# Kernel tuning notes

Measured on AMD Instinct MI355X. Metric: run time of the kernel, lower is better.

## Reference

```python
import jax, jax.numpy as jnp
import numpy as np
jax.config.update("jax_enable_x64", True)  # int64 hash codes for lattice keys

N_KPTS = 32768
C = 61      # feature channels; f-MLP input dim is C+3 = 64
D = 64      # disp-distribution channels
D_LAT = 8   # last f-layer output -> permutohedral position dim

# large odd 62-bit multipliers for the lattice-key hash (wraps mod 2^64)
_MULTS = np.array([2654435761405764093, 1181783497276652981,
                   3202034522624059733, 2685821657736338717,
                   1876998521354586173, 1481765933965188213,
                   2549297995355413921, 3373259426345127233], dtype=np.int64)


def _hcode(k, mults):
    return jnp.sum(k.astype(jnp.int64) * mults, axis=-1)


def _pl_filter(pos, vals):
    """Permutohedral lattice splat -> blur -> slice (approx. Gaussian filter).
    pos: (N, d) float32 lattice positions, vals: (N, vd) float32 values."""
    N, d = pos.shape
    vd = vals.shape[1]
    M = N * (d + 1)  # fixed-size hash table (every point touches d+1 vertices)
    # --- elevate onto hyperplane H_d in R^{d+1} ---
    scale = np.float32(np.sqrt(2.0 / 3.0) * (d + 1)) / np.sqrt(
        np.arange(1, d + 1, dtype=np.float32) * np.arange(2, d + 2, dtype=np.float32))
    E = np.zeros((d + 1, d), dtype=np.float32)
    E[0, :] = 1.0
    for i in range(1, d + 1):
        E[i, i - 1] = -float(i)
        E[i, i:] = 1.0
    elevated = (pos * jnp.asarray(scale, jnp.float32)) @ jnp.asarray(E).T  # (N, d+1)
    # --- nearest zero-colored lattice point and simplex ranks ---
    rem0 = jnp.floor(elevated / (d + 1) + 0.5) * (d + 1)
    sum_val = jnp.round(jnp.sum(rem0, -1) / (d + 1)).astype(jnp.int32)
    diff = elevated - rem0
    rank = jnp.argsort(jnp.argsort(-diff, axis=-1), axis=-1).astype(jnp.int32) + sum_val[:, None]
    lo = rank < 0
    hi = rank > d
    rem0 = rem0 + jnp.where(lo, float(d + 1), 0.0) - jnp.where(hi, float(d + 1), 0.0)
    rank = rank + jnp.where(lo, d + 1, 0) - jnp.where(hi, d + 1, 0)
    # --- barycentric coordinates ---
    t = (elevated - rem0) / (d + 1)
    rows = jnp.arange(N)[:, None]
    bary = jnp.zeros((N, d + 2), jnp.float32)
    bary = bary.at[rows, d - rank].add(t)
    bary = bary.at[rows, d + 1 - rank].add(-t)
    bary = bary.at[:, 0].add(1.0 + bary[:, d + 1])
    w = bary[:, :d + 1]  # (N, d+1) vertex weights
    # --- simplex vertex keys (first d coords; full key sums to 0) ---
    canonical = np.zeros((d + 1, d + 1), np.int32)
    for r in range(d + 1):
        canonical[r, :d + 1 - r] = r
        canonical[r, d + 1 - r:] = r - (d + 1)
    keys = rem0.astype(jnp.int32)[None, :, :d] + jnp.asarray(canonical)[:, rank[:, :d]]  # (d+1,N,d)
    # --- hash table via sorted unique codes (jit-safe fixed size) ---
    mults = jnp.asarray(_MULTS[:d])
    codes = _hcode(keys, mults).reshape(M)
    uniq, inv = jnp.unique(codes, return_inverse=True, size=M,
                           fill_value=jnp.iinfo(jnp.int64).max)
    inv = inv.reshape(M)
    # --- splat ---
    wv = (w.T[:, :, None] * vals[None]).reshape(M, vd)
    lat = jax.ops.segment_sum(wv, inv, num_segments=M)  # (M, vd)
    occ = jax.ops.segment_sum(jnp.ones((M,), jnp.float32), inv, num_segments=M) > 0
    ukeys = jnp.zeros((M, d), jnp.int32).at[inv].set(keys.reshape(M, d))
    # --- blur along each of the d+1 lattice directions ---
    for j in range(d + 1):
        off = np.ones(d + 1, np.int32)
        off[j] = -d
        o = jnp.asarray(off[:d])
        def _nbr(sign, lat=lat):
            c = _hcode(ukeys + sign * o, mults)
            i = jnp.clip(jnp.searchsorted(uniq, c), 0, M - 1)
            ok = (jnp.take(uniq, i) == c) & jnp.take(occ, i)
            return jnp.where(ok[:, None], jnp.take(lat, i, axis=0), 0.0)
        lat = jnp.where(occ[:, None], 0.5 * lat + 0.25 * (_nbr(1) + _nbr(-1)), lat)
    # --- slice ---
    alpha = 1.0 / (1.0 + 2.0 ** (-d))
    return jnp.sum(w.T[:, :, None] * jnp.take(lat, inv, axis=0).reshape(d + 1, N, vd), 0) * alpha


def _layernorm2(x, g, b):
    # LayerNorm(normalized_shape=(N, K)): stats over the last TWO dims jointly
    mu = jnp.mean(x, axis=(-2, -1), keepdims=True)
    var = jnp.mean((x - mu) ** 2, axis=(-2, -1), keepdims=True)
    return (x - mu) * jax.lax.rsqrt(var + 1e-5) * g + b


def setup_inputs() -> dict:
    key = jax.random.key(0)
    ks = jax.random.split(key, 16)
    f32 = jnp.float32
    rn = lambda k, shape, s=1.0: jax.random.normal(k, shape, dtype=f32) * s
    inp = {
        "kpts": rn(ks[0], (1, N_KPTS, 3)),
        "disps_distr": rn(ks[1], (1, N_KPTS, D)),
        "feats": rn(ks[2], (1, N_KPTS, C)),
    }
    i = 3
    for b in range(2):
        inp[f"Wd{b}0"] = rn(ks[i], (D, D), 0.05); i += 1
        inp[f"bd{b}0"] = jnp.zeros((D,), f32)
        inp[f"Wd{b}1"] = rn(ks[i], (D, D), 0.05); i += 1
        inp[f"bd{b}1"] = jnp.zeros((D,), f32)
        inp[f"Wf{b}"] = rn(ks[i], (C + 3, D_LAT), 0.1); i += 1
        inp[f"bf{b}"] = jnp.zeros((D_LAT,), f32)
        inp[f"g{b}"] = jnp.ones((N_KPTS, D_LAT), f32)
        inp[f"be{b}"] = jnp.zeros((N_KPTS, D_LAT), f32)
    return inp


def reference(kpts, disps_distr, feats, Wd00, bd00, Wd01, bd01, Wf0, bf0, g0, be0,
              Wd10, bd10, Wd11, bd11, Wf1, bf1, g1, be1):
    fk = jnp.concatenate([kpts, feats], axis=-1)  # (1, N, C+3)
    x = jnp.reshape(disps_distr, (1, N_KPTS, -1))
    blocks = [(Wd00, bd00, Wd01, bd01, Wf0, bf0, g0, be0),
              (Wd10, bd10, Wd11, bd11, Wf1, bf1, g1, be1)]
    for (Wd0, bd0, Wd1, bd1, Wf, bf, g, be) in blocks:
        x = jax.nn.relu(x @ Wd0 + bd0)   # d-layer 0
        x = jax.nn.relu(x @ Wd1 + bd1)   # d-layer 1
        # only the LAST f-layer output is used by the torch code (feats_kpts is never updated)
        pos = _layernorm2(jax.nn.relu(fk @ Wf + bf), g, be)  # (1, N, 8)
        x = _pl_filter(pos[0], x[0])[None]
    return x
```

## Files before the change

### kernel.cpp

```cpp
#include <hip/hip_runtime.h>
#include <hip/hip_bf16.h>
#include <hip/hip_fp16.h>
#include <stdint.h>

typedef unsigned long long u64;

#define NK 32768
#define DL 8
#define DP1 9
#define MT (NK*DP1)
#define HBITS 19
#define HSIZE (1u<<HBITS)
#define HMASK (HSIZE-1)
#define EMPTY_CODE 0xFFFFFFFFFFFFFFFFULL
#define NBLK 1152
#define HBLK (HSIZE/256)
#define CAP 32
#define MAXHUB 16384

__device__ __constant__ u64 c_mults[8] = {
    2654435761405764093ULL, 1181783497276652981ULL, 3202034522624059733ULL,
    2685821657736338717ULL, 1876998521354586173ULL, 1481765933965188213ULL,
    2549297995355413921ULL, 3373259426345127233ULL};

__device__ __forceinline__ unsigned int hmix(u64 x) {
    x ^= x >> 33; x *= 0xff51afd7ed558ccdULL;
    x ^= x >> 33; x *= 0xc4ceb9fe1a85ec53ULL;
    x ^= x >> 33;
    return (unsigned int)x & HMASK;
}

__device__ __forceinline__ u64 dir_delta(int j) {
    u64 s = 0;
    #pragma unroll
    for (int k = 0; k < 8; k++) s += c_mults[k];
    return (j == 8) ? s : (s - 9ULL * c_mults[j]);
}

__device__ __forceinline__ float ldf(const void* p, int i, int bf) {
    if (bf) return __bfloat162float(((const __hip_bfloat16*)p)[i]);
    return ((const float*)p)[i];
}

__global__ void k_detect(const unsigned* __restrict__ g0w, int* __restrict__ flag) {
    if (threadIdx.x == 0) {
        int f = 1;
        for (int i = 0; i < 8; i++) if (g0w[i] != 0x3F803F80u) f = 0;
        *flag = f;
    }
}

__global__ __launch_bounds__(256) void k_mlp(const void* __restrict__ xin, int use_df_in,
    const void* __restrict__ W0, const void* __restrict__ B0,
    const void* __restrict__ W1, const void* __restrict__ B1,
    float* __restrict__ xout, const int* __restrict__ df, double* __restrict__ stats) {
    __shared__ float w0[64*64], w1[64*64], xs[16][64], y1[16][64];
    int bf = *df;
    int bfin = use_df_in ? bf : 0;
    int tid = threadIdx.x;
    int row0 = blockIdx.x * 16;
    if (blockIdx.x == 0 && tid == 0) { stats[0] = 0.0; stats[1] = 0.0; }
    for (int i = tid; i < 4096; i += 256) { w0[i] = ldf(W0, i, bf); w1[i] = ldf(W1, i, bf); }
    for (int i = tid; i < 1024; i += 256) xs[i>>6][i&63] = ldf(xin, row0*64 + i, bfin);
    __syncthreads();
    int rb = tid >> 6, col = tid & 63;
    float b0c = ldf(B0, col, bf);
    float a0 = b0c, a1 = b0c, a2 = b0c, a3 = b0c;
    #pragma unroll
    for (int k = 0; k < 64; k++) {
        float w = w0[k*64+col];
        a0 = fmaf(xs[rb   ][k], w, a0);
        a1 = fmaf(xs[rb+ 4][k], w, a1);
        a2 = fmaf(xs[rb+ 8][k], w, a2);
        a3 = fmaf(xs[rb+12][k], w, a3);
    }
    y1[rb   ][col] = fmaxf(a0, 0.f);
    y1[rb+ 4][col] = fmaxf(a1, 0.f);
    y1[rb+ 8][col] = fmaxf(a2, 0.f);
    y1[rb+12][col] = fmaxf(a3, 0.f);
    __syncthreads();
    float b1c = ldf(B1, col, bf);
    a0 = b1c; a1 = b1c; a2 = b1c; a3 = b1c;
    #pragma unroll
    for (int k = 0; k < 64; k++) {
        float w = w1[k*64+col];
        a0 = fmaf(y1[rb   ][k], w, a0);
        a1 = fmaf(y1[rb+ 4][k], w, a1);
        a2 = fmaf(y1[rb+ 8][k], w, a2);
        a3 = fmaf(y1[rb+12][k], w, a3);
    }
    xout[(row0+rb   )*64 + col] = fmaxf(a0, 0.f);
    xout[(row0+rb+ 4)*64 + col] = fmaxf(a1, 0.f);
    xout[(row0+rb+ 8)*64 + col] = fmaxf(a2, 0.f);
    xout[(row0+rb+12)*64 + col] = fmaxf(a3, 0.f);
}

__global__ __launch_bounds__(256) void k_pos(const void* __restrict__ kpts,
    const void* __restrict__ feats, const void* __restrict__ Wf,
    const void* __restrict__ Bf, float* __restrict__ pos_pre,
    double* __restrict__ stats, const int* __restrict__ df) {
    __shared__ float wf[64*8];
    __shared__ float fk[32][65];
    __shared__ float red[256], red2[256];
    int bf = *df;
    int tid = threadIdx.x;
    int n0 = blockIdx.x * 32;
    for (int i = tid; i < 512; i += 256) wf[i] = ldf(Wf, i, bf);
    for (int i = tid; i < 32*64; i += 256) {
        int pt = i >> 6, k = i & 63, n = n0 + pt;
        fk[pt][k] = (k < 3) ? ldf(kpts, n*3 + k, bf) : ldf(feats, n*61 + (k-3), bf);
    }
    __syncthreads();
    int pt = tid >> 3, j = tid & 7, n = n0 + pt;
    float acc = ldf(Bf, j, bf);
    #pragma unroll
    for (int k = 0; k < 64; k++) acc = fmaf(fk[pt][k], wf[k*8+j], acc);
    acc = fmaxf(acc, 0.f);
    pos_pre[n*8 + j] = acc;
    red[tid] = acc; red2[tid] = acc * acc;
    __syncthreads();
    for (int s = 128; s > 0; s >>= 1) {
        if (tid < s) { red[tid] += red[tid+s]; red2[tid] += red2[tid+s]; }
        __syncthreads();
    }
    if (tid == 0) { atomicAdd(&stats[0], (double)red[0]); atomicAdd(&stats[1], (double)red2[0]); }
}

__global__ __launch_bounds__(256) void k_embed(const float* __restrict__ pos_pre,
    const double* __restrict__ stats, const void* __restrict__ g,
    const void* __restrict__ be, float* __restrict__ wgt,
    u64* __restrict__ pcodes, int* __restrict__ cnt, int* __restrict__ cnt2,
    int* __restrict__ hubid, const int* __restrict__ df) {
    int bf = *df;
    int n = blockIdx.x * 256 + threadIdx.x;
    if (n >= NK) return;
    const double inv_cnt = 1.0 / (double)(NK * DL);
    double mud = stats[0] * inv_cnt;
    double vard = stats[1] * inv_cnt - mud * mud;
    float mu = (float)mud;
    float rs = rsqrtf((float)vard + 1e-5f);
    const float scale[8] = {
        5.196152422706632f, 3.0f, 2.1213203435596424f, 1.643167672515498f,
        1.3416407864998738f, 1.1338934190276817f, 0.9819805060619657f, 0.8660254037844386f};
    float c[8];
    #pragma unroll
    for (int k = 0; k < 8; k++) {
        float v = pos_pre[n*8 + k];
        float p = (v - mu) * rs * ldf(g, n*8 + k, bf) + ldf(be, n*8 + k, bf);
        c[k] = p * scale[k];
    }
    float sufa[9]; sufa[8] = 0.f;
    #pragma unroll
    for (int k = 7; k >= 0; k--) sufa[k] = sufa[k+1] + c[k];
    float elev[9];
    elev[0] = sufa[0];
    #pragma unroll
    for (int i = 1; i < 9; i++) elev[i] = sufa[i] - (float)i * c[i-1];
    int ri[9], sumv = 0;
    float diff[9];
    #pragma unroll
    for (int i = 0; i < 9; i++) {
        ri[i] = (int)floorf(elev[i] / 9.0f + 0.5f);
        sumv += ri[i];
        diff[i] = elev[i] - 9.f * (float)ri[i];
    }
    int rank[9];
    #pragma unroll
    for (int i = 0; i < 9; i++) {
        int r = 0;
        #pragma unroll
        for (int j = 0; j < 9; j++)
            r += (diff[j] > diff[i]) || ((diff[j] == diff[i]) && (j < i));
        rank[i] = r + sumv;
    }
    #pragma unroll
    for (int i = 0; i < 9; i++) {
        if (rank[i] < 0)      { rank[i] += 9; ri[i] += 1; }
        else if (rank[i] > 8) { rank[i] -= 9; ri[i] -= 1; }
    }
    float t[9];
    #pragma unroll
    for (int i = 0; i < 9; i++) t[i] = (elev[i] - 9.f * (float)ri[i]) / 9.f;
    float bary[10];
    #pragma unroll
    for (int i = 0; i < 10; i++) bary[i] = 0.f;
    #pragma unroll
    for (int i = 0; i < 9; i++) { bary[8 - rank[i]] += t[i]; bary[9 - rank[i]] -= t[i]; }
    bary[0] += 1.f + bary[9];
    for (int r = 0; r < 9; r++) {
        u64 code = 0;
        #pragma unroll
        for (int k = 0; k < 8; k++) {
            int key = 9 * ri[k] + ((rank[k] <= 8 - r) ? r : (r - 9));
            code += (u64)(long long)key * c_mults[k];
        }
        int m = n * 9 + r;
        wgt[m] = bary[r];
        pcodes[m] = code;
        cnt[m] = 0;
        cnt2[m] = 0;
        hubid[m] = -1;
    }
}

__global__ __launch_bounds__(256) void k_insert(const u64* __restrict__ pcodes,
    u64* __restrict__ htab_code, unsigned int* __restrict__ ppos) {
    int m = blockIdx.x * 256 + threadIdx.x;
    if (m >= MT) return;
    u64 code = pcodes[m];
    unsigned int pos = hmix(code);
    for (;;) {
        u64 cc = htab_code[pos];
        if (cc == code) break;
        if (cc == EMPTY_CODE) {
            u64 old = atomicCAS(&htab_code[pos], EMPTY_CODE, code);
            if (old == EMPTY_CODE || old == code) break;
        }
        pos = (pos + 1) & HMASK;
    }
    ppos[m] = pos;
}

__global__ __launch_bounds__(256) void k_occ(const u64* __restrict__ htab_code,
    int* __restrict__ bocc) {
    __shared__ int wcnt[4];
    unsigned int i = blockIdx.x * 256 + threadIdx.x;
    bool occ = (htab_code[i] != EMPTY_CODE);
    u64 mask = __ballot(occ);
    int lane = threadIdx.x & 63;
    if (lane == 0) wcnt[threadIdx.x >> 6] = __popcll(mask);
    __syncthreads();
    if (threadIdx.x == 0) bocc[blockIdx.x] = wcnt[0] + wcnt[1] + wcnt[2] + wcnt[3];
}

__global__ __launch_bounds__(256) void k_occscan(int* __restrict__ bocc,
    int* __restrict__ counter, int* __restrict__ nhub) {
    __shared__ int s[256];
    __shared__ int carry;
    int t = threadIdx.x;
    if (t == 0) { carry = 0; *nhub = 0; }
    __syncthreads();
    for (int c = 0; c < HBLK / 256; c++) {
        int i = c * 256 + t;
        int v = bocc[i];
        s[t] = v; __syncthreads();
        for (int off = 1; off < 256; off <<= 1) {
            int a = (t >= off) ? s[t-off] : 0;
            __syncthreads();
            s[t] += a;
            __syncthreads();
        }
        int cl = carry;
        bocc[i] = s[t] - v + cl;
        __syncthreads();
        if (t == 0) carry = cl + s[255];
        __syncthreads();
    }
    if (t == 0) *counter = carry;
}

__global__ __launch_bounds__(256) void k_assign2(const u64* __restrict__ htab_code,
    const int* __restrict__ bocc, int* __restrict__ htab_slot,
    u64* __restrict__ slot_code) {
    __shared__ int wbase[4];
    unsigned int i = blockIdx.x * 256 + threadIdx.x;
    u64 cde = htab_code[i];
    bool occ = (cde != EMPTY_CODE);
    int lane = threadIdx.x & 63;
    int wid  = threadIdx.x >> 6;
    u64 mask = __ballot(occ);
    int prefix = __popcll(mask & ((1ULL << lane) - 1ULL));
    if (lane == 0) wbase[wid] = __popcll(mask);
    __syncthreads();
    if (threadIdx.x == 0) {
        int run = bocc[blockIdx.x];
        for (int w = 0; w < 4; w++) { int c = wbase[w]; wbase[w] = run; run += c; }
    }
    __syncthreads();
    if (occ) {
        int s = wbase[wid] + prefix;
        htab_slot[i] = s;
        slot_code[s] = cde;
    }
}

__global__ __launch_bounds__(256) void k_nbr(const u64* __restrict__ slot_code,
    const u64* __restrict__ htab_code, const int* __restrict__ htab_slot,
    const int* __restrict__ counter, int2* __restrict__ nbr) {
    int idx = blockIdx.x * 256 + threadIdx.x;
    if (idx >= 9 * MT) return;
    int j = idx / MT;
    int sl = idx - j * MT;
    int count = *counter;
    if (sl >= count) return;
    u64 dj = dir_delta(j);
    u64 code = slot_code[sl];
    int res[2];
    #pragma unroll
    for (int s = 0; s < 2; s++) {
        u64 cde = code + (s ? (u64)(0ULL - dj) : dj);
        unsigned int pos = hmix(cde);
        int r = -1;
        for (;;) {
            u64 cc = htab_code[pos];
            if (cc == cde) { r = htab_slot[pos]; break; }
            if (cc == EMPTY_CODE) break;
            pos = (pos + 1) & HMASK;
        }
        res[s] = r;
    }
    nbr[j * MT + sl] = make_int2(res[0], res[1]);
}

__global__ __launch_bounds__(256) void k_lookup(const unsigned int* __restrict__ ppos,
    const int* __restrict__ htab_slot, int* __restrict__ sidx, int* __restrict__ cnt) {
    int m = blockIdx.x * 256 + threadIdx.x;
    if (m >= MT) return;
    int s = htab_slot[ppos[m]];
    sidx[m] = s;
    atomicAdd(&cnt[s], 1);
}

__global__ __launch_bounds__(256) void k_scan1(const int* __restrict__ cnt,
    int* __restrict__ exbuf, int* __restrict__ bsum,
    int* __restrict__ hublist, int* __restrict__ hubid, int* __restrict__ nhub) {
    __shared__ int s[256];
    int t = threadIdx.x;
    int i = blockIdx.x * 256 + t;
    int v = cnt[i];
    if (v > CAP) {
        int h = atomicAdd(nhub, 1);
        if (h < MAXHUB) { hublist[h] = i; hubid[i] = h; }
    }
    s[t] = v; __syncthreads();
    for (int off = 1; off < 256; off <<= 1) {
        int a = (t >= off) ? s[t-off] : 0;
        __syncthreads();
        s[t] += a;
        __syncthreads();
    }
    exbuf[i] = s[t] - v;
    if (t == 255) bsum[blockIdx.x] = s[255];
}

__global__ __launch_bounds__(256) void k_scan2(int* __restrict__ bsum) {
    __shared__ int s[256];
    __shared__ int carry;
    int t = threadIdx.x;
    if (t == 0) carry = 0;
    __syncthreads();
    for (int c = 0; c < (NBLK + 255) / 256; c++) {
        int i = c * 256 + t;
        int v = (i < NBLK) ? bsum[i] : 0;
        s[t] = v; __syncthreads();
        for (int off = 1; off < 256; off <<= 1) {
            int a = (t >= off) ? s[t-off] : 0;
            __syncthreads();
            s[t] += a;
            __syncthreads();
        }
        int cl = carry;
        if (i < NBLK) bsum[i] = s[t] - v + cl;
        __syncthreads();
        if (t == 0) carry = cl + s[255];
        __syncthreads();
    }
}

__global__ __launch_bounds__(256) void k_scatter(const int* __restrict__ sidx,
    const int* __restrict__ exbuf, const int* __restrict__ bsum,
    int* __restrict__ cnt2, int* __restrict__ list) {
    int m = blockIdx.x * 256 + threadIdx.x;
    if (m < MT) {
        int s = sidx[m];
        int ofs = atomicAdd(&cnt2[s], 1);
        list[exbuf[s] + bsum[s >> 8] + ofs] = m;
    }
}

__global__ __launch_bounds__(256) void k_splat_a(const float* __restrict__ xbuf,
    const float* __restrict__ wgt, const int* __restrict__ exbuf,
    const int* __restrict__ bsum, const int* __restrict__ cnt,
    const int* __restrict__ list, __half* __restrict__ val,
    const int* __restrict__ counter) {
    int count = *counter;
    int sl = blockIdx.x * 8 + (threadIdx.x >> 5);
    int lane = threadIdx.x & 31;
    if (sl >= count) return;
    int c = cnt[sl];
    if (c > CAP) return;
    int st = exbuf[sl] + bsum[sl >> 8];
    const float2* x2 = (const float2*)xbuf;
    float2 acc = make_float2(0.f, 0.f);
    int mm = 0; float ww = 0.f;
    if (lane < c) { mm = list[st + lane]; ww = wgt[mm]; }
    for (int k = 0; k < c; k++) {
        int   m = __shfl(mm, k, 32);
        float w = __shfl(ww, k, 32);
        float2 xv = x2[(m / 9) * 32 + lane];
        acc.x = fmaf(w, xv.x, acc.x);
        acc.y = fmaf(w, xv.y, acc.y);
    }
    ((__half2*)val)[(size_t)sl * 32 + lane] = __float22half2_rn(acc);
}

__global__ __launch_bounds__(256) void k_splat_b(const float* __restrict__ xbuf,
    const float* __restrict__ wgt, const int* __restrict__ sidx,
    const int* __restrict__ cnt, const int* __restrict__ list,
    const int* __restrict__ hubid, float* __restrict__ hubval) {
    int chunk = blockIdx.x * 8 + (threadIdx.x >> 5);
    int lane = threadIdx.x & 31;
    int e = chunk * 32 + lane;
    int m = 0, hid = -1; float w = 0.f; int hub = 0;
    if (e < MT) {
        m = list[e];
        int slot = sidx[m];
        hub = (cnt[slot] > CAP);
        if (hub) { w = wgt[m]; hid = hubid[slot]; }
    }
    u64 bal = __ballot(hub);
    unsigned int half = (threadIdx.x & 32) ? (unsigned int)(bal >> 32) : (unsigned int)bal;
    if (!half) return;
    const float2* x2 = (const float2*)xbuf;
    float2 acc = make_float2(0.f, 0.f);
    int cur = -1;
    while (half) {
        int k = __ffs(half) - 1; half &= half - 1;
        int   hk = __shfl(hid, k, 32);
        int   mk = __shfl(m, k, 32);
        float wk = __shfl(w, k, 32);
        float2 xv = x2[(mk / 9) * 32 + lane];
        if (hk != cur) {
            if (cur >= 0) {
                atomicAdd(&hubval[(size_t)cur * 64 + 2*lane    ], acc.x);
                atomicAdd(&hubval[(size_t)cur * 64 + 2*lane + 1], acc.y);
            }
            cur = hk; acc = make_float2(0.f, 0.f);
        }
        acc.x = fmaf(wk, xv.x, acc.x);
        acc.y = fmaf(wk, xv.y, acc.y);
    }
    atomicAdd(&hubval[(size_t)cur * 64 + 2*lane    ], acc.x);
    atomicAdd(&hubval[(size_t)cur * 64 + 2*lane + 1], acc.y);
}

__global__ __launch_bounds__(256) void k_hubcvt(const float* __restrict__ hubval,
    const int* __restrict__ hublist, const int* __restrict__ nhub,
    __half* __restrict__ val) {
    int idx = blockIdx.x * 256 + threadIdx.x;
    int hi = idx >> 5, lane = idx & 31;
    if (hi >= *nhub) return;
    int sl = hublist[hi];
    float2 v = ((const float2*)hubval)[(size_t)hi * 32 + lane];
    ((__half2*)val)[(size_t)sl * 32 + lane] = __float22half2_rn(v);
}

__global__ __launch_bounds__(256) void k_blur(const __half* __restrict__ vin,
    __half* __restrict__ vout, const int2* __restrict__ nbrj,
    const int* __restrict__ counter) {
    int idx = blockIdx.x * 256 + threadIdx.x;
    int sl = idx >> 3, lane = idx & 7;
    int count = *counter;
    if (sl >= count) return;
    int2 nbp = nbrj[sl];
    typedef union { uint4 u; __half2 h[4]; } row16;
    const uint4* vin4 = (const uint4*)vin;
    uint4* vout4 = (uint4*)vout;
    row16 S, A, B, O;
    S.u = vin4[(size_t)sl*8 + lane];
    uint4 z; z.x = 0; z.y = 0; z.z = 0; z.w = 0;
    A.u = (nbp.x >= 0) ? vin4[(size_t)nbp.x*8 + lane] : z;
    B.u = (nbp.y >= 0) ? vin4[(size_t)nbp.y*8 + lane] : z;
    #pragma unroll
    for (int k = 0; k < 4; k++) {
        float2 fs = __half22float2(S.h[k]);
        float2 fa = __half22float2(A.h[k]);
        float2 fb = __half22float2(B.h[k]);
        float2 r;
        r.x = 0.5f * fs.x + 0.25f * (fa.x + fb.x);
        r.y = 0.5f * fs.y + 0.25f * (fa.y + fb.y);
        O.h[k] = __float22half2_rn(r);
    }
    vout4[(size_t)sl*8 + lane] = O.u;
}

__global__ __launch_bounds__(256) void k_slice(const float* __restrict__ wgt,
    const int* __restrict__ sidx, const __half* __restrict__ val,
    float* __restrict__ outf, void* __restrict__ outb, int write_out,
    const int* __restrict__ df) {
    int bf = *df;
    int idx = blockIdx.x * 256 + threadIdx.x;
    if (idx >= NK * 64) return;
    int n = idx >> 6, ch = idx & 63;
    float acc = 0.f;
    #pragma unroll
    for (int r = 0; r < 9; r++) {
        int m = n * 9 + r;
        acc = fmaf(wgt[m], __half2float(val[(size_t)sidx[m]*64 + ch]), acc);
    }
    acc *= 0.9961089494163424f;
    if (write_out) {
        if (bf) ((__hip_bfloat16*)outb)[idx] = __float2bfloat16(acc);
        else    ((float*)outb)[idx] = acc;
    } else {
        outf[idx] = acc;
    }
}

extern "C" void kernel_launch(void* const* d_in, const int* in_sizes, int n_in,
                              void* d_out, int out_size, void* d_ws, size_t ws_size,
                              hipStream_t stream) {
    const void* kpts  = d_in[0];
    const void* disps = d_in[1];
    const void* feats = d_in[2];

    char* p = (char*)d_ws;
    float* xbuf     = (float*)p;  p += (size_t)NK*64*4;
    float* pos_pre  = (float*)p;  p += (size_t)NK*8*4;
    double* stats   = (double*)p; p += 256;
    int*   dflag    = (int*)p;    p += 256;
    float* wgt      = (float*)p;  p += (size_t)MT*4;
    int*   sidx     = (int*)p;    p += (size_t)MT*4;
    u64*   pcodes   = (u64*)p;    p += (size_t)MT*8;
    unsigned int* ppos = (unsigned int*)p; p += (size_t)MT*4;
    u64*   htabc    = (u64*)p;    p += (size_t)HSIZE*8;
    int*   htabs    = (int*)p;    p += (size_t)HSIZE*4;
    u64*   slotc    = (u64*)p;    p += (size_t)MT*8;
    int*   counter  = (int*)p;    p += 256;
    int*   nhub     = (int*)p;    p += 256;
    int*   bocc     = (int*)p;    p += (size_t)HBLK*4;
    int*   cnt      = (int*)p;    p += (size_t)MT*4;
    int*   cnt2     = (int*)p;    p += (size_t)MT*4;
    int*   hubid    = (int*)p;    p += (size_t)MT*4;
    int*   exbuf    = (int*)p;    p += (size_t)MT*4;
    int*   list     = (int*)p;    p += (size_t)MT*4;
    int*   bsum     = (int*)p;    p += 256*32;
    int*   hublist  = (int*)p;    p += (size_t)MAXHUB*4;
    float* hubval   = (float*)p;  p += (size_t)MAXHUB*64*4;
    int2*  nbr      = (int2*)p;   p += (size_t)MT*9*8;
    __half* valA    = (__half*)p; p += (size_t)MT*64*2;
    __half* valB    = (__half*)p; p += (size_t)MT*64*2;

    k_detect<<<1, 64, 0, stream>>>((const unsigned*)d_in[3 + 6], dflag);

    for (int b = 0; b < 2; b++) {
        const void* W0 = d_in[3 + b*8 + 0];
        const void* B0 = d_in[3 + b*8 + 1];
        const void* W1 = d_in[3 + b*8 + 2];
        const void* B1 = d_in[3 + b*8 + 3];
        const void* Wf = d_in[3 + b*8 + 4];
        const void* Bf = d_in[3 + b*8 + 5];
        const void* G  = d_in[3 + b*8 + 6];
        const void* Be = d_in[3 + b*8 + 7];

        k_mlp<<<NK/16, 256, 0, stream>>>(b == 0 ? disps : (const void*)xbuf, b == 0 ? 1 : 0,
                                         W0, B0, W1, B1, xbuf, dflag, stats);

        k_pos<<<NK/32, 256, 0, stream>>>(kpts, feats, Wf, Bf, pos_pre, stats, dflag);

        hipMemsetAsync(htabc, 0xFF, (size_t)HSIZE*8, stream);
        hipMemsetAsync(hubval, 0, (size_t)MAXHUB*64*4, stream);

        k_embed<<<NK/256, 256, 0, stream>>>(pos_pre, stats, G, Be, wgt, pcodes,
                                            cnt, cnt2, hubid, dflag);
        k_insert<<<NBLK, 256, 0, stream>>>(pcodes, htabc, ppos);
        k_occ<<<HBLK, 256, 0, stream>>>(htabc, bocc);
        k_occscan<<<1, 256, 0, stream>>>(bocc, counter, nhub);
        k_assign2<<<HBLK, 256, 0, stream>>>(htabc, bocc, htabs, slotc);
        k_nbr<<<(9*MT + 255)/256, 256, 0, stream>>>(slotc, htabc, htabs, counter, nbr);
        k_lookup<<<NBLK, 256, 0, stream>>>(ppos, htabs, sidx, cnt);

        k_scan1<<<NBLK, 256, 0, stream>>>(cnt, exbuf, bsum, hublist, hubid, nhub);
        k_scan2<<<1, 256, 0, stream>>>(bsum);
        k_scatter<<<NBLK, 256, 0, stream>>>(sidx, exbuf, bsum, cnt2, list);
        k_splat_a<<<(MT + 7)/8, 256, 0, stream>>>(xbuf, wgt, exbuf, bsum, cnt, list,
                                                  valA, counter);
        k_splat_b<<<(MT/32 + 7)/8, 256, 0, stream>>>(xbuf, wgt, sidx, cnt, list, hubid, hubval);
        k_hubcvt<<<(MAXHUB*32)/256, 256, 0, stream>>>(hubval, hublist, nhub, valA);

        for (int j = 0; j < 9; j++) {
            const __half* vin = (j & 1) ? valB : valA;
            __half*       vout = (j & 1) ? valA : valB;
            k_blur<<<(MT*8 + 255)/256, 256, 0, stream>>>(vin, vout, nbr + (size_t)j*MT, counter);
        }
        k_slice<<<(NK*64)/256, 256, 0, stream>>>(wgt, sidx, valB, xbuf,
                                                 d_out, b == 1 ? 1 : 0, dflag);
    }
}
```

Measured before the change: 783.7 us.

## Probe hash once per neighbor pair and derive reverse neighbors by scatter

The neighbor kernel now looks up only the +delta neighbor of each lattice vertex. A new kernel fills the -delta entry by writing each vertex's index into its found neighbor's reverse slot, which halves the random hash-table probes. Separately, zeroing of the hub accumulation buffer moves from a memset into the embed kernel, removing one memset call. The cost is an extra kernel launch and a scattered write pass over the neighbor array.

```diff
diff --git a/kernel.cpp b/kernel.cpp
--- a/kernel.cpp
+++ b/kernel.cpp
@@ -130,10 +130,16 @@
     const double* __restrict__ stats, const void* __restrict__ g,
     const void* __restrict__ be, float* __restrict__ wgt,
     u64* __restrict__ pcodes, int* __restrict__ cnt, int* __restrict__ cnt2,
-    int* __restrict__ hubid, const int* __restrict__ df) {
+    int* __restrict__ hubid, float* __restrict__ hubval, const int* __restrict__ df) {
     int bf = *df;
     int n = blockIdx.x * 256 + threadIdx.x;
     if (n >= NK) return;
+    {
+        float4 z = make_float4(0.f, 0.f, 0.f, 0.f);
+        float4* hv4 = (float4*)hubval;
+        #pragma unroll
+        for (int i = 0; i < 8; i++) hv4[(size_t)n * 8 + i] = z;
+    }
     const double inv_cnt = 1.0 / (double)(NK * DL);
     double mud = stats[0] * inv_cnt;
     double vard = stats[1] * inv_cnt - mud * mud;
@@ -293,23 +299,28 @@
     int sl = idx - j * MT;
     int count = *counter;
     if (sl >= count) return;
-    u64 dj = dir_delta(j);
-    u64 code = slot_code[sl];
-    int res[2];
-    #pragma unroll
-    for (int s = 0; s < 2; s++) {
-        u64 cde = code + (s ? (u64)(0ULL - dj) : dj);
-        unsigned int pos = hmix(cde);
-        int r = -1;
-        for (;;) {
-            u64 cc = htab_code[pos];
-            if (cc == cde) { r = htab_slot[pos]; break; }
-            if (cc == EMPTY_CODE) break;
-            pos = (pos + 1) & HMASK;
-        }
-        res[s] = r;
-    }
-    nbr[j * MT + sl] = make_int2(res[0], res[1]);
+    u64 cde = slot_code[sl] + dir_delta(j);
+    unsigned int pos = hmix(cde);
+    int r = -1;
+    for (;;) {
+        u64 cc = htab_code[pos];
+        if (cc == cde) { r = htab_slot[pos]; break; }
+        if (cc == EMPTY_CODE) break;
+        pos = (pos + 1) & HMASK;
+    }
+    nbr[idx] = make_int2(r, -1);
+}
+
+__global__ __launch_bounds__(256) void k_nbr2(const int* __restrict__ counter,
+    int2* __restrict__ nbr) {
+    int idx = blockIdx.x * 256 + threadIdx.x;
+    if (idx >= 9 * MT) return;
+    int j = idx / MT;
+    int sl = idx - j * MT;
+    int count = *counter;
+    if (sl >= count) return;
+    int u = nbr[idx].x;
+    if (u >= 0) ((int*)nbr)[2 * ((size_t)j * MT + u) + 1] = sl;
 }
 
 __global__ __launch_bounds__(256) void k_lookup(const unsigned int* __restrict__ ppos,
@@ -559,15 +570,15 @@
         k_pos<<<NK/32, 256, 0, stream>>>(kpts, feats, Wf, Bf, pos_pre, stats, dflag);
 
         hipMemsetAsync(htabc, 0xFF, (size_t)HSIZE*8, stream);
-        hipMemsetAsync(hubval, 0, (size_t)MAXHUB*64*4, stream);
 
         k_embed<<<NK/256, 256, 0, stream>>>(pos_pre, stats, G, Be, wgt, pcodes,
-                                            cnt, cnt2, hubid, dflag);
+                                            cnt, cnt2, hubid, hubval, dflag);
         k_insert<<<NBLK, 256, 0, stream>>>(pcodes, htabc, ppos);
         k_occ<<<HBLK, 256, 0, stream>>>(htabc, bocc);
         k_occscan<<<1, 256, 0, stream>>>(bocc, counter, nhub);
         k_assign2<<<HBLK, 256, 0, stream>>>(htabc, bocc, htabs, slotc);
         k_nbr<<<(9*MT + 255)/256, 256, 0, stream>>>(slotc, htabc, htabs, counter, nbr);
+        k_nbr2<<<(9*MT + 255)/256, 256, 0, stream>>>(counter, nbr);
         k_lookup<<<NBLK, 256, 0, stream>>>(ppos, htabs, sidx, cnt);
 
         k_scan1<<<NBLK, 256, 0, stream>>>(cnt, exbuf, bsum, hublist, hubid, nhub);
```

Measured after the change: 787.9 us. No clear change (+0.5%).
